# Kernel optimization log

Hardware: AMD Instinct MI355X
Metric: run time of the kernel (lower is better)

## Reference

```python
import jax, jax.numpy as jnp
import numpy as np

B, H, I, T_MAX = 8192, 1024, 128, 128

def setup_inputs() -> dict:
    key = jax.random.key(0)
    k1, k2, k3, k4, k5 = jax.random.split(key, 5)
    s = 1.0 / np.sqrt(I + H)
    return {
        "t": jnp.asarray(37.5, dtype=jnp.float32),
        "h": jax.random.normal(k1, (B, H), dtype=jnp.float32),
        "x_coeffs": jax.random.normal(k2, (T_MAX, B, I), dtype=jnp.float32),
        "W_r": jax.random.normal(k3, (H, I + H), dtype=jnp.float32) * s,
        "W_z": jax.random.normal(k4, (H, I + H), dtype=jnp.float32) * s,
        "W_h": jax.random.normal(k5, (H, I + H), dtype=jnp.float32) * s,
    }

def reference(t, h, x_coeffs, W_r, W_z, W_h):
    time_max = x_coeffs.shape[0]
    t_int = jnp.clip(t.astype(jnp.int32), 0, time_max - 1)
    x = x_coeffs[t_int]                                   # [B, I]
    combined = jnp.concatenate([x, h], axis=1)            # [B, I+H]
    r = jax.nn.sigmoid(combined @ W_r.T)                  # [B, H]
    z = jax.nn.sigmoid(combined @ W_z.T)                  # [B, H]
    combined_rh = jnp.concatenate([x, r * h], axis=1)     # [B, I+H]
    h_tilde = jnp.tanh(combined_rh @ W_h.T)               # [B, H]
    dh = (1.0 - z) * (h_tilde - h)
    return dh
```

## Files before the change

kernel.cpp:

```cpp
#include <hip/hip_runtime.h>
#include <hip/hip_bf16.h>
#include <stdint.h>

#define B_ROWS 8192
#define HDIM   1024
#define IDIM   128
#define KDIM   1152
#define TMAX   128

typedef unsigned short u16;
typedef __bf16 bf16x8 __attribute__((ext_vector_type(8)));
typedef float  f32x4  __attribute__((ext_vector_type(4)));

static __device__ __forceinline__ u16 f2bf(float f) {
  union { float f; unsigned u; } v; v.f = f;
  unsigned r = v.u + 0x7FFFu + ((v.u >> 16) & 1u);
  return (u16)(r >> 16);
}
static __device__ __forceinline__ float bf2f(u16 b) {
  union { unsigned u; float f; } v; v.u = ((unsigned)b) << 16; return v.f;
}

template<int N> __device__ __forceinline__ void waitv() {
  if constexpr (N == 8)      asm volatile("s_waitcnt vmcnt(8)" ::: "memory");
  else if constexpr (N == 6) asm volatile("s_waitcnt vmcnt(6)" ::: "memory");
  else if constexpr (N == 2) asm volatile("s_waitcnt vmcnt(2)" ::: "memory");
  else                       asm volatile("s_waitcnt vmcnt(0)" ::: "memory");
}

#define W_CHUNKS  (3*1024*1152/4)
#define H_CHUNKS  (B_ROWS*HDIM/4)
#define X_CHUNKS  (B_ROWS*IDIM/4)
#define W_BLOCKS  (W_CHUNKS/256)
#define H_BLOCKS  (H_CHUNKS/256)
#define X_BLOCKS  (X_CHUNKS/256)
#define CV_BLOCKS (W_BLOCKS + H_BLOCKS + X_BLOCKS)

__global__ __launch_bounds__(256)
void convert_kernel(const float* __restrict__ t,
                    const float* __restrict__ h,
                    const float* __restrict__ xc,
                    const float* __restrict__ Wr,
                    const float* __restrict__ Wz,
                    const float* __restrict__ Wh,
                    u16* __restrict__ WB,
                    u16* __restrict__ A1)
{
  const int b = blockIdx.x;
  const int tid = threadIdx.x;
  if (b < W_BLOCKS) {
    const int g = b * 256 + tid;
    const int e = g * 4;
    const int S = 1024 * KDIM;
    float4 v;
    if (e < S)            v = *reinterpret_cast<const float4*>(Wr + e);
    else if (e < 2 * S)   v = *reinterpret_cast<const float4*>(Wz + (e - S));
    else                  v = *reinterpret_cast<const float4*>(Wh + (e - 2 * S));
    ushort4 o; o.x = f2bf(v.x); o.y = f2bf(v.y); o.z = f2bf(v.z); o.w = f2bf(v.w);
    *reinterpret_cast<ushort4*>(WB + e) = o;
  } else if (b < W_BLOCKS + H_BLOCKS) {
    const int g = (b - W_BLOCKS) * 256 + tid;
    const int e = g * 4;
    const int row = e >> 10, col = e & 1023;
    float4 v = *reinterpret_cast<const float4*>(h + e);
    ushort4 o; o.x = f2bf(v.x); o.y = f2bf(v.y); o.z = f2bf(v.z); o.w = f2bf(v.w);
    *reinterpret_cast<ushort4*>(A1 + (size_t)row * KDIM + IDIM + col) = o;
  } else {
    const int g = (b - W_BLOCKS - H_BLOCKS) * 256 + tid;
    const int e = g * 4;
    int ti = (int)t[0];
    ti = ti < 0 ? 0 : (ti > TMAX - 1 ? TMAX - 1 : ti);
    const int row = e >> 7, col = e & 127;
    float4 v = *reinterpret_cast<const float4*>(xc + (size_t)ti * B_ROWS * IDIM + e);
    ushort4 o; o.x = f2bf(v.x); o.y = f2bf(v.y); o.z = f2bf(v.z); o.w = f2bf(v.w);
    *reinterpret_cast<ushort4*>(A1 + (size_t)row * KDIM + col) = o;
  }
}

__global__ __launch_bounds__(256, 2)
void gemm1_256(const u16* __restrict__ A, const u16* __restrict__ W,
               const u16* __restrict__ hb, u16* __restrict__ A2w,
               u16* __restrict__ omz)
{
  constexpr int NBN  = 2048 / 128;
  constexpr int BMPX = 32 / 8;
  constexpr int NT   = KDIM / 32;

  __shared__ u16 As[3][256 * 32];
  __shared__ u16 Bs[3][128 * 32];

  const int tid  = threadIdx.x;
  const int lane = tid & 63;
  const int wave = tid >> 6;
  const int wm = wave >> 1, wn = wave & 1;
  const int xcd = blockIdx.x & 7, jj = blockIdx.x >> 3;
  const int bm = xcd * BMPX + (jj & (BMPX - 1));
  const int bn = jj / BMPX;
  const int rowBase = bm * 256, colBase = bn * 128;
  const int lr = lane & 15, lkq = lane >> 4;

  auto stage = [&](int slot, int kt) {
    #pragma unroll
    for (int rr = 0; rr < 4; ++rr) {
      const int q = rr * 256 + tid;
      const int row = q >> 2, pc = q & 3;
      const int cg = pc ^ ((row >> 1) & 3);
      const u16* g = A + (size_t)(rowBase + row) * KDIM + kt * 32 + cg * 8;
      __builtin_amdgcn_global_load_lds(
          (const __attribute__((address_space(1))) void*)g,
          (__attribute__((address_space(3))) void*)(&As[slot][q * 8]), 16, 0, 0);
    }
    #pragma unroll
    for (int rr = 0; rr < 2; ++rr) {
      const int q = rr * 256 + tid;
      const int row = q >> 2, pc = q & 3;
      const int cg = pc ^ ((row >> 1) & 3);
      const u16* g = W + (size_t)(colBase + row) * KDIM + kt * 32 + cg * 8;
      __builtin_amdgcn_global_load_lds(
          (const __attribute__((address_space(1))) void*)g,
          (__attribute__((address_space(3))) void*)(&Bs[slot][q * 8]), 16, 0, 0);
    }
  };

  f32x4 acc[8][4];
  f32x4 zero = {0.f, 0.f, 0.f, 0.f};
  #pragma unroll
  for (int i = 0; i < 8; ++i)
    #pragma unroll
    for (int j = 0; j < 4; ++j) acc[i][j] = zero;

#define PHASE1(T, DOSTAGE, WV)  do {                                            \
    if (DOSTAGE) stage((T + 2) % 3, (T) + 2);                                   \
    const int s_ = (T) % 3;                                                     \
    bf16x8 af[8], bv[4];                                                        \
    _Pragma("unroll") for (int mf = 0; mf < 8; ++mf) {                          \
      const int r = wm * 128 + mf * 16 + lr;                                    \
      const int c = lkq ^ ((r >> 1) & 3);                                       \
      af[mf] = *reinterpret_cast<const bf16x8*>(&As[s_][r * 32 + c * 8]);       \
    }                                                                           \
    _Pragma("unroll") for (int nf = 0; nf < 4; ++nf) {                          \
      const int r = wn * 64 + nf * 16 + lr;                                     \
      const int c = lkq ^ ((r >> 1) & 3);                                       \
      bv[nf] = *reinterpret_cast<const bf16x8*>(&Bs[s_][r * 32 + c * 8]);       \
    }                                                                           \
    __builtin_amdgcn_s_barrier();                                               \
    asm volatile("s_waitcnt lgkmcnt(0)" ::: "memory");                          \
    __builtin_amdgcn_s_setprio(1);                                              \
    _Pragma("unroll") for (int mf = 0; mf < 8; ++mf)                            \
      _Pragma("unroll") for (int nf = 0; nf < 4; ++nf)                          \
        acc[mf][nf] = __builtin_amdgcn_mfma_f32_16x16x32_bf16(                  \
            af[mf], bv[nf], acc[mf][nf], 0, 0, 0);                              \
    __builtin_amdgcn_s_setprio(0);                                              \
    waitv<WV>();                                                                \
    __builtin_amdgcn_s_barrier();                                               \
  } while (0)

  stage(0, 0); stage(1, 1);
  waitv<6>();
  __builtin_amdgcn_s_barrier();

  for (int t = 0; t < NT - 2; ++t) PHASE1(t, true, 6);
  PHASE1(NT - 2, false, 0);
  PHASE1(NT - 1, false, 0);
#undef PHASE1

  if (colBase < HDIM) {
    #pragma unroll
    for (int mf = 0; mf < 8; ++mf)
      #pragma unroll
      for (int nf = 0; nf < 4; ++nf) {
        f32x4 v = acc[mf][nf];
        const int col = colBase + wn * 64 + nf * 16 + lr;
        #pragma unroll
        for (int rr = 0; rr < 4; ++rr) {
          const int row = rowBase + wm * 128 + mf * 16 + lkq * 4 + rr;
          const float sg = 1.f / (1.f + __expf(-v[rr]));
          const float hv = bf2f(hb[(size_t)row * KDIM + IDIM + col]);
          A2w[(size_t)row * KDIM + IDIM + col] = f2bf(sg * hv);
        }
      }
  } else {
    #pragma unroll
    for (int mf = 0; mf < 8; ++mf)
      #pragma unroll
      for (int nf = 0; nf < 4; ++nf) {
        f32x4 v = acc[mf][nf];
        const int col = colBase - HDIM + wn * 64 + nf * 16 + lr;
        #pragma unroll
        for (int rr = 0; rr < 4; ++rr) {
          const int row = rowBase + wm * 128 + mf * 16 + lkq * 4 + rr;
          const float sg = 1.f / (1.f + __expf(-v[rr]));
          omz[(size_t)row * HDIM + col] = f2bf(1.f - sg);
        }
      }
  }
}

__global__ __launch_bounds__(256, 2)
void gemm2_128(const u16* __restrict__ A, const u16* __restrict__ Ax,
               const u16* __restrict__ W,
               const u16* __restrict__ hb, const u16* __restrict__ omz,
               float* __restrict__ out)
{
  constexpr int NBN  = 1024 / 128;
  constexpr int BMPX = (B_ROWS / 128) / 8;
  constexpr int NT   = KDIM / 64;

  __shared__ u16 As[2][2][64 * 64];
  __shared__ u16 Bs[2][2][64 * 64];

  const int tid  = threadIdx.x;
  const int lane = tid & 63;
  const int wave = tid >> 6;
  const int wm = wave >> 1, wn = wave & 1;
  const int xcd = blockIdx.x & 7, jj = blockIdx.x >> 3;
  const int bm = xcd * BMPX + (jj & (BMPX - 1));
  const int bn = jj / BMPX;
  const int rowBase = bm * 128, colBase = bn * 128;
  const int lr = lane & 15, lkq = lane >> 4;

  auto stA = [&](int buf, int half, int kt) {
    const u16* src = (kt * 64 < IDIM) ? Ax : A;
    #pragma unroll
    for (int rr = 0; rr < 2; ++rr) {
      const int q = rr * 256 + tid;
      const int row = q >> 3, cl = q & 7;
      const int cg = cl ^ (row & 7);
      const u16* g = src + (size_t)(rowBase + half * 64 + row) * KDIM + kt * 64 + cg * 8;
      __builtin_amdgcn_global_load_lds(
          (const __attribute__((address_space(1))) void*)g,
          (__attribute__((address_space(3))) void*)(&As[buf][half][q * 8]), 16, 0, 0);
    }
  };
  auto stB = [&](int buf, int half, int kt) {
    #pragma unroll
    for (int rr = 0; rr < 2; ++rr) {
      const int q = rr * 256 + tid;
      const int row = q >> 3, cl = q & 7;
      const int cg = cl ^ (row & 7);
      const u16* g = W + (size_t)(colBase + half * 64 + row) * KDIM + kt * 64 + cg * 8;
      __builtin_amdgcn_global_load_lds(
          (const __attribute__((address_space(1))) void*)g,
          (__attribute__((address_space(3))) void*)(&Bs[buf][half][q * 8]), 16, 0, 0);
    }
  };

  f32x4 acc[2][2][2][2];
  f32x4 zero = {0.f, 0.f, 0.f, 0.f};
  #pragma unroll
  for (int a = 0; a < 2; ++a)
    #pragma unroll
    for (int b = 0; b < 2; ++b)
      #pragma unroll
      for (int c = 0; c < 2; ++c)
        #pragma unroll
        for (int d = 0; d < 2; ++d) acc[a][b][c][d] = zero;

  bf16x8 bv[2][2][2];
  bf16x8 af[2][2];

  auto rdA = [&](int buf, int half) {
    #pragma unroll
    for (int mf = 0; mf < 2; ++mf)
      #pragma unroll
      for (int kk = 0; kk < 2; ++kk) {
        const int r = wm * 32 + mf * 16 + lr;
        const int c = (kk * 4 + lkq) ^ (r & 7);
        af[mf][kk] = *reinterpret_cast<const bf16x8*>(&As[buf][half][r * 64 + c * 8]);
      }
  };
  auto rdB = [&](int buf) {
    #pragma unroll
    for (int nh = 0; nh < 2; ++nh)
      #pragma unroll
      for (int nf = 0; nf < 2; ++nf)
        #pragma unroll
        for (int kk = 0; kk < 2; ++kk) {
          const int r = wn * 32 + nf * 16 + lr;
          const int c = (kk * 4 + lkq) ^ (r & 7);
          bv[nh][nf][kk] = *reinterpret_cast<const bf16x8*>(&Bs[buf][nh][r * 64 + c * 8]);
        }
  };

#define MFMA_QUAD(MH, NH)                                                       \
    _Pragma("unroll") for (int mf = 0; mf < 2; ++mf)                            \
      _Pragma("unroll") for (int nf = 0; nf < 2; ++nf)                          \
        _Pragma("unroll") for (int kk = 0; kk < 2; ++kk)                        \
          acc[MH][NH][mf][nf] = __builtin_amdgcn_mfma_f32_16x16x32_bf16(        \
              af[mf][kk], bv[NH][nf][kk], acc[MH][NH][mf][nf], 0, 0, 0);

#define PHASE_A(BUF, T, DO_STAGE, WV)  do {                                     \
    rdA(BUF, 0); rdB(BUF);                                                      \
    if (DO_STAGE) stA((BUF) ^ 1, 1, (T) + 1);                                   \
    __builtin_amdgcn_s_barrier();                                               \
    asm volatile("s_waitcnt lgkmcnt(0)" ::: "memory");                          \
    __builtin_amdgcn_s_setprio(1);                                              \
    MFMA_QUAD(0, 0); MFMA_QUAD(0, 1);                                           \
    __builtin_amdgcn_s_setprio(0);                                              \
    waitv<WV>();                                                                \
    __builtin_amdgcn_s_barrier();                                               \
  } while (0)

#define PHASE_B(BUF, T, DO_STAGE, WV)  do {                                     \
    rdA(BUF, 1);                                                                \
    if (DO_STAGE) { stA(BUF, 0, (T) + 2); stB(BUF, 0, (T) + 2);                 \
                    stB(BUF, 1, (T) + 2); }                                     \
    __builtin_amdgcn_s_barrier();                                               \
    asm volatile("s_waitcnt lgkmcnt(0)" ::: "memory");                          \
    __builtin_amdgcn_s_setprio(1);                                              \
    MFMA_QUAD(1, 1); MFMA_QUAD(1, 0);                                           \
    __builtin_amdgcn_s_setprio(0);                                              \
    waitv<WV>();                                                                \
    __builtin_amdgcn_s_barrier();                                               \
  } while (0)

  stA(0, 0, 0); stB(0, 0, 0); stB(0, 1, 0); stA(0, 1, 0);
  stA(1, 0, 1); stB(1, 0, 1); stB(1, 1, 1);
  waitv<6>();
  __builtin_amdgcn_s_barrier();

  for (int t = 0; t < NT - 2; ++t) {
    const int buf = t & 1;
    PHASE_A(buf, t, true, 8);
    PHASE_B(buf, t, true, 8);
  }
  PHASE_A(0, 16, true, 8);
  PHASE_B(0, 16, false, 2);
  PHASE_A(1, 17, false, 0);
  PHASE_B(1, 17, false, 0);

#undef PHASE_A
#undef PHASE_B
#undef MFMA_QUAD

  #pragma unroll
  for (int mh = 0; mh < 2; ++mh)
    #pragma unroll
    for (int nh = 0; nh < 2; ++nh)
      #pragma unroll
      for (int mf = 0; mf < 2; ++mf)
        #pragma unroll
        for (int nf = 0; nf < 2; ++nf) {
          f32x4 v = acc[mh][nh][mf][nf];
          const int col = colBase + nh * 64 + wn * 32 + nf * 16 + lr;
          #pragma unroll
          for (int rr = 0; rr < 4; ++rr) {
            const int row = rowBase + mh * 64 + wm * 32 + mf * 16 + lkq * 4 + rr;
            const float e  = __expf(2.f * v[rr]);
            const float ht = 1.f - 2.f / (e + 1.f);
            const float o  = bf2f(omz[(size_t)row * HDIM + col]);
            const float hv = bf2f(hb[(size_t)row * KDIM + IDIM + col]);
            out[(size_t)row * HDIM + col] = o * (ht - hv);
          }
        }
}

extern "C" void kernel_launch(void* const* d_in, const int* in_sizes, int n_in,
                              void* d_out, int out_size, void* d_ws, size_t ws_size,
                              hipStream_t stream) {
  const float* t  = (const float*)d_in[0];
  const float* h  = (const float*)d_in[1];
  const float* xc = (const float*)d_in[2];
  const float* Wr = (const float*)d_in[3];
  const float* Wz = (const float*)d_in[4];
  const float* Wh = (const float*)d_in[5];
  float* out = (float*)d_out;

  u16* WB  = (u16*)d_ws;
  u16* A1  = WB + (size_t)3 * 1024 * KDIM;
  u16* A2  = A1 + (size_t)B_ROWS * KDIM;
  u16* omz = A2 + (size_t)B_ROWS * KDIM;

  convert_kernel<<<CV_BLOCKS, 256, 0, stream>>>(t, h, xc, Wr, Wz, Wh, WB, A1);

  gemm1_256<<<512, 256, 0, stream>>>(A1, WB, A1, A2, omz);

  gemm2_128<<<512, 256, 0, stream>>>(A2, A1, WB + (size_t)2048 * KDIM,
                                     A1, omz, out);
}
```

Measured before the change: 94.56 us.

## Enlarge gate GEMM tile to 256x256 with 512 threads and BK=64 double buffering

Replaces the 256x128 output tile (256 threads, 3-stage pipeline, BK=32) in the first GEMM with a 256x256 tile computed by 8 waves. K steps are 64 wide, use double buffering and an 8-way XOR swizzle, and the grid shrinks to 256 blocks. The larger tile raises arithmetic intensity and cuts redundant global and LDS traffic for A and W. In exchange it uses 128KB of LDS per block, which allows only one block per CU, and a shallower pipeline that waits on all loads every iteration, so latency hiding gets worse.

```diff
diff --git a/kernel.cpp b/kernel.cpp
--- a/kernel.cpp
+++ b/kernel.cpp
@@ -77,48 +77,48 @@
   }
 }
 
-__global__ __launch_bounds__(256, 2)
-void gemm1_256(const u16* __restrict__ A, const u16* __restrict__ W,
-               const u16* __restrict__ hb, u16* __restrict__ A2w,
-               u16* __restrict__ omz)
+__global__ __launch_bounds__(512, 2)
+void gemm1_256sq(const u16* __restrict__ A, const u16* __restrict__ W,
+                 const u16* __restrict__ hb, u16* __restrict__ A2w,
+                 u16* __restrict__ omz)
 {
-  constexpr int NBN  = 2048 / 128;
+  constexpr int NBN  = 2048 / 256;
   constexpr int BMPX = 32 / 8;
-  constexpr int NT   = KDIM / 32;
-
-  __shared__ u16 As[3][256 * 32];
-  __shared__ u16 Bs[3][128 * 32];
+  constexpr int NT   = KDIM / 64;
+
+  __shared__ u16 As[2][256 * 64];
+  __shared__ u16 Bs[2][256 * 64];
 
   const int tid  = threadIdx.x;
   const int lane = tid & 63;
   const int wave = tid >> 6;
-  const int wm = wave >> 1, wn = wave & 1;
+  const int wm = wave >> 2, wn = wave & 3;
   const int xcd = blockIdx.x & 7, jj = blockIdx.x >> 3;
   const int bm = xcd * BMPX + (jj & (BMPX - 1));
-  const int bn = jj / BMPX;
-  const int rowBase = bm * 256, colBase = bn * 128;
+  const int bn = jj >> 2;
+  const int rowBase = bm * 256, colBase = bn * 256;
   const int lr = lane & 15, lkq = lane >> 4;
 
-  auto stage = [&](int slot, int kt) {
+  auto stage = [&](int buf, int kt) {
     #pragma unroll
     for (int rr = 0; rr < 4; ++rr) {
-      const int q = rr * 256 + tid;
-      const int row = q >> 2, pc = q & 3;
-      const int cg = pc ^ ((row >> 1) & 3);
-      const u16* g = A + (size_t)(rowBase + row) * KDIM + kt * 32 + cg * 8;
+      const int q = rr * 512 + tid;
+      const int row = q >> 3, cl = q & 7;
+      const int cg = cl ^ (row & 7);
+      const u16* g = A + (size_t)(rowBase + row) * KDIM + kt * 64 + cg * 8;
       __builtin_amdgcn_global_load_lds(
           (const __attribute__((address_space(1))) void*)g,
-          (__attribute__((address_space(3))) void*)(&As[slot][q * 8]), 16, 0, 0);
-    }
-    #pragma unroll
-    for (int rr = 0; rr < 2; ++rr) {
-      const int q = rr * 256 + tid;
-      const int row = q >> 2, pc = q & 3;
-      const int cg = pc ^ ((row >> 1) & 3);
-      const u16* g = W + (size_t)(colBase + row) * KDIM + kt * 32 + cg * 8;
+          (__attribute__((address_space(3))) void*)(&As[buf][q * 8]), 16, 0, 0);
+    }
+    #pragma unroll
+    for (int rr = 0; rr < 4; ++rr) {
+      const int q = rr * 512 + tid;
+      const int row = q >> 3, cl = q & 7;
+      const int cg = cl ^ (row & 7);
+      const u16* g = W + (size_t)(colBase + row) * KDIM + kt * 64 + cg * 8;
       __builtin_amdgcn_global_load_lds(
           (const __attribute__((address_space(1))) void*)g,
-          (__attribute__((address_space(3))) void*)(&Bs[slot][q * 8]), 16, 0, 0);
+          (__attribute__((address_space(3))) void*)(&Bs[buf][q * 8]), 16, 0, 0);
     }
   };
 
@@ -129,40 +129,59 @@
     #pragma unroll
     for (int j = 0; j < 4; ++j) acc[i][j] = zero;
 
-#define PHASE1(T, DOSTAGE, WV)  do {                                            \
-    if (DOSTAGE) stage((T + 2) % 3, (T) + 2);                                   \
-    const int s_ = (T) % 3;                                                     \
-    bf16x8 af[8], bv[4];                                                        \
-    _Pragma("unroll") for (int mf = 0; mf < 8; ++mf) {                          \
-      const int r = wm * 128 + mf * 16 + lr;                                    \
-      const int c = lkq ^ ((r >> 1) & 3);                                       \
-      af[mf] = *reinterpret_cast<const bf16x8*>(&As[s_][r * 32 + c * 8]);       \
-    }                                                                           \
-    _Pragma("unroll") for (int nf = 0; nf < 4; ++nf) {                          \
-      const int r = wn * 64 + nf * 16 + lr;                                     \
-      const int c = lkq ^ ((r >> 1) & 3);                                       \
-      bv[nf] = *reinterpret_cast<const bf16x8*>(&Bs[s_][r * 32 + c * 8]);       \
-    }                                                                           \
-    __builtin_amdgcn_s_barrier();                                               \
-    asm volatile("s_waitcnt lgkmcnt(0)" ::: "memory");                          \
-    __builtin_amdgcn_s_setprio(1);                                              \
-    _Pragma("unroll") for (int mf = 0; mf < 8; ++mf)                            \
-      _Pragma("unroll") for (int nf = 0; nf < 4; ++nf)                          \
-        acc[mf][nf] = __builtin_amdgcn_mfma_f32_16x16x32_bf16(                  \
-            af[mf], bv[nf], acc[mf][nf], 0, 0, 0);                              \
-    __builtin_amdgcn_s_setprio(0);                                              \
-    waitv<WV>();                                                                \
-    __builtin_amdgcn_s_barrier();                                               \
-  } while (0)
-
-  stage(0, 0); stage(1, 1);
-  waitv<6>();
+  stage(0, 0);
+  waitv<0>();
   __builtin_amdgcn_s_barrier();
 
-  for (int t = 0; t < NT - 2; ++t) PHASE1(t, true, 6);
-  PHASE1(NT - 2, false, 0);
-  PHASE1(NT - 1, false, 0);
-#undef PHASE1
+  for (int t = 0; t < NT; ++t) {
+    const int buf = t & 1;
+    bf16x8 af[8], bv[4];
+    #pragma unroll
+    for (int mf = 0; mf < 8; ++mf) {
+      const int r = wm * 128 + mf * 16 + lr;
+      const int c = lkq ^ (r & 7);
+      af[mf] = *reinterpret_cast<const bf16x8*>(&As[buf][r * 64 + c * 8]);
+    }
+    #pragma unroll
+    for (int nf = 0; nf < 4; ++nf) {
+      const int r = wn * 64 + nf * 16 + lr;
+      const int c = lkq ^ (r & 7);
+      bv[nf] = *reinterpret_cast<const bf16x8*>(&Bs[buf][r * 64 + c * 8]);
+    }
+    if (t + 1 < NT) stage(buf ^ 1, t + 1);
+    asm volatile("s_waitcnt lgkmcnt(0)" ::: "memory");
+    __builtin_amdgcn_s_setprio(1);
+    #pragma unroll
+    for (int mf = 0; mf < 8; ++mf)
+      #pragma unroll
+      for (int nf = 0; nf < 4; ++nf)
+        acc[mf][nf] = __builtin_amdgcn_mfma_f32_16x16x32_bf16(
+            af[mf], bv[nf], acc[mf][nf], 0, 0, 0);
+    __builtin_amdgcn_s_setprio(0);
+    #pragma unroll
+    for (int mf = 0; mf < 8; ++mf) {
+      const int r = wm * 128 + mf * 16 + lr;
+      const int c = (4 + lkq) ^ (r & 7);
+      af[mf] = *reinterpret_cast<const bf16x8*>(&As[buf][r * 64 + c * 8]);
+    }
+    #pragma unroll
+    for (int nf = 0; nf < 4; ++nf) {
+      const int r = wn * 64 + nf * 16 + lr;
+      const int c = (4 + lkq) ^ (r & 7);
+      bv[nf] = *reinterpret_cast<const bf16x8*>(&Bs[buf][r * 64 + c * 8]);
+    }
+    asm volatile("s_waitcnt lgkmcnt(0)" ::: "memory");
+    __builtin_amdgcn_s_setprio(1);
+    #pragma unroll
+    for (int mf = 0; mf < 8; ++mf)
+      #pragma unroll
+      for (int nf = 0; nf < 4; ++nf)
+        acc[mf][nf] = __builtin_amdgcn_mfma_f32_16x16x32_bf16(
+            af[mf], bv[nf], acc[mf][nf], 0, 0, 0);
+    __builtin_amdgcn_s_setprio(0);
+    waitv<0>();
+    __builtin_amdgcn_s_barrier();
+  }
 
   if (colBase < HDIM) {
     #pragma unroll
@@ -373,7 +392,7 @@
 
   convert_kernel<<<CV_BLOCKS, 256, 0, stream>>>(t, h, xc, Wr, Wz, Wh, WB, A1);
 
-  gemm1_256<<<512, 256, 0, stream>>>(A1, WB, A1, A2, omz);
+  gemm1_256sq<<<256, 512, 0, stream>>>(A1, WB, A1, A2, omz);
 
   gemm2_128<<<512, 256, 0, stream>>>(A2, A1, WB + (size_t)2048 * KDIM,
                                      A1, omz, out);
```

Measured after the change: 87.62 us. 1.08x faster.
